# Kernel optimization log

Hardware: AMD Instinct MI355X
Metric: run time of the kernel (lower is better)

Reference implementation:

```python
import jax, jax.numpy as jnp
import numpy as np

N_U, N_P, E, E_LAB = 100000, 50000, 2000000, 500000
D_U, D_P, H = 64, 128, 64


def _seg_mean(feat, idx, n):
    # scatter-mean: sum per destination / clamp(count, 1)
    s = jax.ops.segment_sum(feat, idx, num_segments=n)
    c = jax.ops.segment_sum(jnp.ones((idx.shape[0],), feat.dtype), idx, num_segments=n)
    return s / jnp.maximum(c, 1.0)[:, None]


def setup_inputs() -> dict:
    key = jax.random.key(0)
    ks = jax.random.split(key, 16)
    inp = {
        'x_user': jax.random.normal(ks[0], (N_U, D_U), jnp.float32),
        'x_product': jax.random.normal(ks[1], (N_P, D_P), jnp.float32),
        'W1_buys_l': jax.random.normal(ks[2], (D_U, H), jnp.float32) * 0.05,
        'b1_buys': jnp.zeros((H,), jnp.float32),
        'W1_buys_r': jax.random.normal(ks[3], (D_P, H), jnp.float32) * 0.05,
        'W1_rev_l': jax.random.normal(ks[4], (D_P, H), jnp.float32) * 0.05,
        'b1_rev': jnp.zeros((H,), jnp.float32),
        'W1_rev_r': jax.random.normal(ks[5], (D_U, H), jnp.float32) * 0.05,
        'W2_buys_l': jax.random.normal(ks[6], (H, H), jnp.float32) * 0.05,
        'b2_buys': jnp.zeros((H,), jnp.float32),
        'W2_buys_r': jax.random.normal(ks[7], (H, H), jnp.float32) * 0.05,
        'W2_rev_l': jax.random.normal(ks[8], (H, H), jnp.float32) * 0.05,
        'b2_rev': jnp.zeros((H,), jnp.float32),
        'W2_rev_r': jax.random.normal(ks[9], (H, H), jnp.float32) * 0.05,
        'edge_src': jax.random.randint(ks[10], (E,), 0, N_U, jnp.int32),
        'edge_dst': jax.random.randint(ks[11], (E,), 0, N_P, jnp.int32),
        'lab_u': jax.random.randint(ks[12], (E_LAB,), 0, N_U, jnp.int32),
        'lab_p': jax.random.randint(ks[13], (E_LAB,), 0, N_P, jnp.int32),
    }
    return inp


def reference(x_user, x_product, W1_buys_l, b1_buys, W1_buys_r, W1_rev_l, b1_rev, W1_rev_r,
              W2_buys_l, b2_buys, W2_buys_r, W2_rev_l, b2_rev, W2_rev_r,
              edge_src, edge_dst, lab_u, lab_p):
    # SAGEConv (mean aggr): out_dst = mean_agg(x_src) @ W_l + b + x_dst @ W_r
    def sage(x_src, x_dst, src, dst, n_dst, Wl, b, Wr):
        agg = _seg_mean(x_src[src], dst, n_dst)
        return agg @ Wl + b + x_dst @ Wr

    n_u, n_p = x_user.shape[0], x_product.shape[0]
    # layer 1 (per edge type, hetero) + relu
    h_p = jax.nn.relu(sage(x_user, x_product, edge_src, edge_dst, n_p, W1_buys_l, b1_buys, W1_buys_r))
    h_u = jax.nn.relu(sage(x_product, x_user, edge_dst, edge_src, n_u, W1_rev_l, b1_rev, W1_rev_r))
    # layer 2
    h_p2 = sage(h_u, h_p, edge_src, edge_dst, n_p, W2_buys_l, b2_buys, W2_buys_r)
    h_u2 = sage(h_p, h_u, edge_dst, edge_src, n_u, W2_rev_l, b2_rev, W2_rev_r)
    # classifier: per-label-edge dot product
    return jnp.sum(h_u2[lab_u] * h_p2[lab_p], axis=-1)
```

## Files before the change

### kernel.cpp

```cpp
#include <hip/hip_runtime.h>


using u16 = unsigned short;
using u32 = unsigned int;

__device__ __forceinline__ u16 bf16r(float f) {
    u32 b = __float_as_uint(f);
    b += 0x7fffu + ((b >> 16) & 1u);
    return (u16)(b >> 16);
}
__device__ __forceinline__ float bflo(u32 u) { return __uint_as_float(u << 16); }
__device__ __forceinline__ float bfhi(u32 u) { return __uint_as_float(u & 0xffff0000u); }

#define BSH 8
#define MAXB 512
#define CHUNK 4096
#define RPT 16
#define HB 512

__global__ __launch_bounds__(256) void k_histCast(const int* __restrict__ esrc,
                                                  const int* __restrict__ edst,
                                                  int* __restrict__ bcntP,
                                                  int* __restrict__ bcntU,
                                                  int NBP, int NBU, int E,
                                                  const float* __restrict__ xc,
                                                  u16* __restrict__ yc, int n8) {
    __shared__ int hP[MAXB];
    __shared__ int hU[MAXB];
    int tid = threadIdx.x;
    if ((int)blockIdx.x >= HB) {
        int i = (blockIdx.x - HB) * 256 + tid;
        if (i < n8) {
            const float4* x4 = (const float4*)xc;
            float4 a = x4[i * 2], b = x4[i * 2 + 1];
            uint4 o;
            o.x = (u32)bf16r(a.x) | ((u32)bf16r(a.y) << 16);
            o.y = (u32)bf16r(a.z) | ((u32)bf16r(a.w) << 16);
            o.z = (u32)bf16r(b.x) | ((u32)bf16r(b.y) << 16);
            o.w = (u32)bf16r(b.z) | ((u32)bf16r(b.w) << 16);
            ((uint4*)yc)[i] = o;
        }
        return;
    }
    for (int i = tid; i < MAXB; i += 256) { hP[i] = 0; hU[i] = 0; }
    __syncthreads();
    int E4 = E >> 2;
    const int4* s4 = (const int4*)esrc;
    const int4* d4 = (const int4*)edst;
    int stride = HB * 256;
    for (int i = blockIdx.x * 256 + tid; i < E4; i += stride) {
        int4 s = s4[i], d = d4[i];
        atomicAdd(&hU[s.x >> BSH], 1); atomicAdd(&hU[s.y >> BSH], 1);
        atomicAdd(&hU[s.z >> BSH], 1); atomicAdd(&hU[s.w >> BSH], 1);
        atomicAdd(&hP[d.x >> BSH], 1); atomicAdd(&hP[d.y >> BSH], 1);
        atomicAdd(&hP[d.z >> BSH], 1); atomicAdd(&hP[d.w >> BSH], 1);
    }
    if (blockIdx.x == 0 && tid < (E & 3)) {
        int e = E4 * 4 + tid;
        atomicAdd(&hU[esrc[e] >> BSH], 1);
        atomicAdd(&hP[edst[e] >> BSH], 1);
    }
    __syncthreads();
    for (int i = tid; i < NBP; i += 256) if (hP[i]) atomicAdd(&bcntP[i], hP[i]);
    for (int i = tid; i < NBU; i += 256) if (hU[i]) atomicAdd(&bcntU[i], hU[i]);
}

__global__ __launch_bounds__(256) void k_scanBuckets(const int* __restrict__ cntP,
                                                     int* __restrict__ basesP,
                                                     int* __restrict__ curP, int NBP,
                                                     const int* __restrict__ cntU,
                                                     int* __restrict__ basesU,
                                                     int* __restrict__ curU, int NBU) {
    const int* cnt; int* bases; int* cur; int NB;
    if (blockIdx.x == 0) { cnt = cntP; bases = basesP; cur = curP; NB = NBP; }
    else                 { cnt = cntU; bases = basesU; cur = curU; NB = NBU; }
    __shared__ int sA[MAXB];
    __shared__ int sB[MAXB];
    int tid = threadIdx.x;
    int v0 = (tid < NB) ? cnt[tid] : 0;
    int v1 = (tid + 256 < NB) ? cnt[tid + 256] : 0;
    sA[tid] = v0; sA[tid + 256] = v1;
    __syncthreads();
    int* src = sA; int* dst = sB;
    for (int off = 1; off < MAXB; off <<= 1) {
        dst[tid] = src[tid] + ((tid >= off) ? src[tid - off] : 0);
        int i2 = tid + 256;
        dst[i2] = src[i2] + ((i2 >= off) ? src[i2 - off] : 0);
        __syncthreads();
        int* t = src; src = dst; dst = t;
    }
    if (tid < NB)       { bases[tid] = src[tid] - v0;             cur[tid] = src[tid] - v0; }
    if (tid + 256 < NB) { bases[tid + 256] = src[tid + 256] - v1; cur[tid + 256] = src[tid + 256] - v1; }
    if (tid == 0) bases[NB] = src[MAXB - 1];
}

__global__ __launch_bounds__(256) void k_partition2(
    const int* __restrict__ keysP, const int* __restrict__ payP,
    int* __restrict__ curPp, uint2* __restrict__ pairsP, int NBP,
    const int* __restrict__ keysU, const int* __restrict__ payU,
    int* __restrict__ curUp, uint2* __restrict__ pairsU, int NBU,
    int E, int pblocks) {
    __shared__ int hist[MAXB];
    __shared__ int sA[MAXB];
    __shared__ int sB[MAXB];
    __shared__ int bx[MAXB];
    __shared__ int gbase[MAXB];
    __shared__ uint2 prs[CHUNK];
    const int* keys; const int* payload; int* cursor; uint2* pairs; int NB, cb;
    if ((int)blockIdx.x < pblocks) {
        keys = keysP; payload = payP; cursor = curPp; pairs = pairsP; NB = NBP;
        cb = blockIdx.x;
    } else {
        keys = keysU; payload = payU; cursor = curUp; pairs = pairsU; NB = NBU;
        cb = blockIdx.x - pblocks;
    }
    int tid = threadIdx.x;
    int i0 = cb * CHUNK;
    int count = min(CHUNK, E - i0);
    for (int i = tid; i < MAXB; i += 256) hist[i] = 0;
    __syncthreads();
    int keyr[RPT], payr[RPT], rankr[RPT];
#pragma unroll
    for (int r = 0; r < RPT; ++r) {
        int idx = r * 256 + tid;
        if (idx < count) {
            int k = keys[i0 + idx];
            keyr[r] = k;
            payr[r] = payload[i0 + idx];
            rankr[r] = atomicAdd(&hist[k >> BSH], 1);
        } else keyr[r] = -1;
    }
    __syncthreads();
    sA[tid] = hist[tid]; sA[tid + 256] = hist[tid + 256];
    __syncthreads();
    int* src = sA; int* dst = sB;
    for (int off = 1; off < MAXB; off <<= 1) {
        dst[tid] = src[tid] + ((tid >= off) ? src[tid - off] : 0);
        int i2 = tid + 256;
        dst[i2] = src[i2] + ((i2 >= off) ? src[i2 - off] : 0);
        __syncthreads();
        int* t = src; src = dst; dst = t;
    }
    bx[tid] = src[tid] - hist[tid];
    bx[tid + 256] = src[tid + 256] - hist[tid + 256];
    __syncthreads();
    for (int b = tid; b < NB; b += 256) {
        int c = hist[b];
        gbase[b] = c ? atomicAdd(&cursor[b], c) : 0;
    }
#pragma unroll
    for (int r = 0; r < RPT; ++r) {
        if (keyr[r] >= 0)
            prs[bx[keyr[r] >> BSH] + rankr[r]] = make_uint2((u32)keyr[r], (u32)payr[r]);
    }
    __syncthreads();
    for (int j = tid; j < count; j += 256) {
        uint2 pr = prs[j];
        int b = pr.x >> BSH;
        pairs[gbase[b] + (j - bx[b])] = pr;
    }
}

__global__ __launch_bounds__(256) void k_bucketFill(
    const uint2* __restrict__ pairsP, const int* __restrict__ basesP, int NBP,
    int* __restrict__ nbr_p, int* __restrict__ deg_p, int* __restrict__ ptr_p, int NP,
    const uint2* __restrict__ pairsU, const int* __restrict__ basesU, int NBU,
    int* __restrict__ nbr_u, int* __restrict__ deg_u, int* __restrict__ ptr_u, int NU) {
    const uint2* pairs; const int* bases; int* nbr; int* deg; int* ptr; int N; int bucket;
    if ((int)blockIdx.x < NBP) {
        pairs = pairsP; bases = basesP; nbr = nbr_p; deg = deg_p; ptr = ptr_p; N = NP;
        bucket = blockIdx.x;
    } else {
        pairs = pairsU; bases = basesU; nbr = nbr_u; deg = deg_u; ptr = ptr_u; N = NU;
        bucket = blockIdx.x - NBP;
    }
    int tid = threadIdx.x;
    int base = bases[bucket];
    int cnt = bases[bucket + 1] - base;
    __shared__ int h[256];
    __shared__ int s[256];
    __shared__ int cur[256];
    h[tid] = 0;
    __syncthreads();
    for (int j = tid; j < cnt; j += 256) atomicAdd(&h[pairs[base + j].x & 255], 1);
    __syncthreads();
    int d = h[tid];
    s[tid] = d;
    __syncthreads();
    for (int off = 1; off < 256; off <<= 1) {
        int v = (tid >= off) ? s[tid - off] : 0;
        __syncthreads();
        s[tid] += v;
        __syncthreads();
    }
    int excl = s[tid] - d;
    int node = bucket * 256 + tid;
    if (node < N) { deg[node] = d; ptr[node] = base + excl; }
    cur[tid] = excl;
    __syncthreads();
    for (int j = tid; j < cnt; j += 256) {
        uint2 pr = pairs[base + j];
        int pos = atomicAdd(&cur[pr.x & 255], 1);
        nbr[base + pos] = (int)(pr.y << 7);
    }
}

#define ACC8(A0,A1,A2,A3,A4,A5,A6,A7,V) \
    A0 += bflo((V).x); A1 += bfhi((V).x); A2 += bflo((V).y); A3 += bfhi((V).y); \
    A4 += bflo((V).z); A5 += bfhi((V).z); A6 += bflo((V).w); A7 += bfhi((V).w);

__global__ __launch_bounds__(256) void k_gather2(
    const u16* __restrict__ yA, const int* __restrict__ nbrA, const int* __restrict__ stpA,
    const int* __restrict__ degA, float* __restrict__ aggA, int NA,
    const u16* __restrict__ yB, const int* __restrict__ nbrB, const int* __restrict__ stpB,
    const int* __restrict__ degB, float* __restrict__ aggB, int NB) {
    int w = (blockIdx.x * 256 + threadIdx.x) >> 6;
    int lane = threadIdx.x & 63;
    if (w >= NA + NB) return;
    const u16* y; const int* nbr; const int* stp; const int* deg; float* agg; int n;
    if (w < NA) { y = yA; nbr = nbrA; stp = stpA; deg = degA; agg = aggA; n = w; }
    else        { y = yB; nbr = nbrB; stp = stpB; deg = degB; agg = aggB; n = w - NA; }
    const int q = lane >> 3, t = lane & 7;
    const int d = deg[n];
    const int st = stp[n];
    const char* yb = (const char*)y + t * 16;
    float a0=0,a1=0,a2=0,a3=0,a4=0,a5=0,a6=0,a7=0;
    for (int j = 0; j < d; j += 64) {
        const int cnt = min(d - j, 64);
        int offv = 0;
        if (lane < cnt) offv = nbr[st + j + lane];
#define GLD(R) \
        int g##R = __shfl(offv, R * 8 + q, 64); \
        uint4 v##R = make_uint4(0u, 0u, 0u, 0u); \
        if (R * 8 + q < cnt) v##R = *(const uint4*)(yb + g##R);
        GLD(0) GLD(1) GLD(2) GLD(3) GLD(4) GLD(5) GLD(6) GLD(7)
#undef GLD
#define ACCR(R) if (R * 8 < cnt) { ACC8(a0,a1,a2,a3,a4,a5,a6,a7,v##R) }
        ACCR(0) ACCR(1) ACCR(2) ACCR(3) ACCR(4) ACCR(5) ACCR(6) ACCR(7)
#undef ACCR
    }
#pragma unroll
    for (int m = 8; m < 64; m <<= 1) {
        a0 += __shfl_xor(a0, m, 64); a1 += __shfl_xor(a1, m, 64);
        a2 += __shfl_xor(a2, m, 64); a3 += __shfl_xor(a3, m, 64);
        a4 += __shfl_xor(a4, m, 64); a5 += __shfl_xor(a5, m, 64);
        a6 += __shfl_xor(a6, m, 64); a7 += __shfl_xor(a7, m, 64);
    }
    if (q == 0) {
        float dinv = 1.0f / (float)max(d, 1);
        float* dstp = agg + n * 64 + t * 8;
        *(float4*)dstp       = make_float4(a0 * dinv, a1 * dinv, a2 * dinv, a3 * dinv);
        *(float4*)(dstp + 4) = make_float4(a4 * dinv, a5 * dinv, a6 * dinv, a7 * dinv);
    }
}

#define FMA_ROW(ACC, O, W4) \
    ACC[0] += (O) * (W4).x; ACC[1] += (O) * (W4).y; \
    ACC[2] += (O) * (W4).z; ACC[3] += (O) * (W4).w;

template <int K, int ROWS, bool RELU, bool EMIT, bool PRE, bool BIAS, bool STORE>
__global__ __launch_bounds__(256) void k_ctile(const float* __restrict__ pre,
                                               const float* __restrict__ bias,
                                               const float* __restrict__ x,
                                               const float* __restrict__ W,
                                               float* __restrict__ h,
                                               u16* __restrict__ hbf, int N) {
    constexpr int RR = ROWS / 16;
    constexpr int STRIDE = K + 4;
    constexpr int KF4 = K / 4;
    __shared__ float Ws[K * 64];
    __shared__ float op[ROWS * STRIDE];
    const int tid = threadIdx.x;
    for (int i = tid; i < K * 16; i += 256)
        ((float4*)Ws)[i] = ((const float4*)W)[i];
    const int c4 = (tid & 15) * 4;
    const int rb = (tid >> 4) * RR;
    float bx_ = 0.f, by_ = 0.f, bz_ = 0.f, bw_ = 0.f;
    if (BIAS) {
        float4 b4 = *(const float4*)(bias + c4);
        bx_ = b4.x; by_ = b4.y; bz_ = b4.z; bw_ = b4.w;
    }
    const int ntiles = (N + ROWS - 1) / ROWS;
    for (int tile = blockIdx.x; tile < ntiles; tile += gridDim.x) {
        const int row0 = tile * ROWS;
        __syncthreads();
        for (int i = tid; i < ROWS * KF4; i += 256) {
            int r = i / KF4, k4 = (i % KF4) * 4;
            int row = row0 + r;
            float4 v = make_float4(0.f, 0.f, 0.f, 0.f);
            if (row < N) v = *(const float4*)(x + (size_t)row * K + k4);
            *(float4*)(op + r * STRIDE + k4) = v;
        }
        __syncthreads();
        float acc[RR][4];
#pragma unroll
        for (int i = 0; i < RR; ++i) {
            float px = 0.f, py = 0.f, pz = 0.f, pw = 0.f;
            if (PRE) {
                int row = row0 + rb + i;
                if (row < N) {
                    float4 p = *(const float4*)(pre + row * 64 + c4);
                    px = p.x; py = p.y; pz = p.z; pw = p.w;
                }
            }
            acc[i][0] = bx_ + px; acc[i][1] = by_ + py;
            acc[i][2] = bz_ + pz; acc[i][3] = bw_ + pw;
        }
        for (int kk = 0; kk < K; kk += 4) {
            float4 w0 = *(const float4*)(Ws + (kk + 0) * 64 + c4);
            float4 w1 = *(const float4*)(Ws + (kk + 1) * 64 + c4);
            float4 w2 = *(const float4*)(Ws + (kk + 2) * 64 + c4);
            float4 w3 = *(const float4*)(Ws + (kk + 3) * 64 + c4);
#pragma unroll
            for (int i = 0; i < RR; ++i) {
                float4 o = *(const float4*)(op + (rb + i) * STRIDE + kk);
                FMA_ROW(acc[i], o.x, w0);
                FMA_ROW(acc[i], o.y, w1);
                FMA_ROW(acc[i], o.z, w2);
                FMA_ROW(acc[i], o.w, w3);
            }
        }
#pragma unroll
        for (int i = 0; i < RR; ++i) {
            int row = row0 + rb + i;
            if (row >= N) continue;
            float v0 = acc[i][0], v1 = acc[i][1], v2 = acc[i][2], v3 = acc[i][3];
            if (RELU) {
                v0 = fmaxf(v0, 0.f); v1 = fmaxf(v1, 0.f);
                v2 = fmaxf(v2, 0.f); v3 = fmaxf(v3, 0.f);
            }
            if (STORE)
                *(float4*)(h + row * 64 + c4) = make_float4(v0, v1, v2, v3);
            if (EMIT) {
                uint2 o;
                o.x = (u32)bf16r(v0) | ((u32)bf16r(v1) << 16);
                o.y = (u32)bf16r(v2) | ((u32)bf16r(v3) << 16);
                *(uint2*)(hbf + row * 64 + c4) = o;
            }
        }
    }
}

template <bool PRE, bool BIAS, bool RELU, bool EMIT>
__global__ __launch_bounds__(256) void k_ctilePair64X(
    const float* __restrict__ pre0, const float* __restrict__ bias0,
    const float* __restrict__ x0, const float* __restrict__ W0,
    float* __restrict__ h0, u16* __restrict__ hbf0, int N0, int g0,
    const float* __restrict__ pre1, const float* __restrict__ bias1,
    const float* __restrict__ x1, const float* __restrict__ W1,
    float* __restrict__ h1, u16* __restrict__ hbf1, int N1) {
    constexpr int ROWS = 64, RR = 4, STRIDE = 68, KF4 = 16;
    __shared__ float Ws[64 * 64];
    __shared__ float op[ROWS * STRIDE];
    const float* pre; const float* bias; const float* x; const float* W;
    float* h; u16* hbf;
    int N, bid, gsz;
    if ((int)blockIdx.x < g0) {
        pre = pre0; bias = bias0; x = x0; W = W0; h = h0; hbf = hbf0; N = N0;
        bid = blockIdx.x; gsz = g0;
    } else {
        pre = pre1; bias = bias1; x = x1; W = W1; h = h1; hbf = hbf1; N = N1;
        bid = blockIdx.x - g0; gsz = gridDim.x - g0;
    }
    const int tid = threadIdx.x;
    for (int i = tid; i < 64 * 16; i += 256)
        ((float4*)Ws)[i] = ((const float4*)W)[i];
    const int c4 = (tid & 15) * 4;
    const int rb = (tid >> 4) * RR;
    float bx_ = 0.f, by_ = 0.f, bz_ = 0.f, bw_ = 0.f;
    if (BIAS) {
        float4 b4 = *(const float4*)(bias + c4);
        bx_ = b4.x; by_ = b4.y; bz_ = b4.z; bw_ = b4.w;
    }
    const int ntiles = (N + ROWS - 1) / ROWS;
    for (int tile = bid; tile < ntiles; tile += gsz) {
        const int row0 = tile * ROWS;
        __syncthreads();
        for (int i = tid; i < ROWS * KF4; i += 256) {
            int r = i / KF4, k4 = (i % KF4) * 4;
            int row = row0 + r;
            float4 v = make_float4(0.f, 0.f, 0.f, 0.f);
            if (row < N) v = *(const float4*)(x + (size_t)row * 64 + k4);
            *(float4*)(op + r * STRIDE + k4) = v;
        }
        __syncthreads();
        float acc[RR][4];
#pragma unroll
        for (int i = 0; i < RR; ++i) {
            float px = 0.f, py = 0.f, pz = 0.f, pw = 0.f;
            if (PRE) {
                int row = row0 + rb + i;
                if (row < N) {
                    float4 p = *(const float4*)(pre + row * 64 + c4);
                    px = p.x; py = p.y; pz = p.z; pw = p.w;
                }
            }
            acc[i][0] = bx_ + px; acc[i][1] = by_ + py;
            acc[i][2] = bz_ + pz; acc[i][3] = bw_ + pw;
        }
        for (int kk = 0; kk < 64; kk += 4) {
            float4 w0 = *(const float4*)(Ws + (kk + 0) * 64 + c4);
            float4 w1 = *(const float4*)(Ws + (kk + 1) * 64 + c4);
            float4 w2 = *(const float4*)(Ws + (kk + 2) * 64 + c4);
            float4 w3 = *(const float4*)(Ws + (kk + 3) * 64 + c4);
#pragma unroll
            for (int i = 0; i < RR; ++i) {
                float4 o = *(const float4*)(op + (rb + i) * STRIDE + kk);
                FMA_ROW(acc[i], o.x, w0);
                FMA_ROW(acc[i], o.y, w1);
                FMA_ROW(acc[i], o.z, w2);
                FMA_ROW(acc[i], o.w, w3);
            }
        }
#pragma unroll
        for (int i = 0; i < RR; ++i) {
            int row = row0 + rb + i;
            if (row >= N) continue;
            float v0 = acc[i][0], v1 = acc[i][1], v2 = acc[i][2], v3 = acc[i][3];
            if (RELU) {
                v0 = fmaxf(v0, 0.f); v1 = fmaxf(v1, 0.f);
                v2 = fmaxf(v2, 0.f); v3 = fmaxf(v3, 0.f);
            }
            *(float4*)(h + row * 64 + c4) = make_float4(v0, v1, v2, v3);
            if (EMIT) {
                uint2 o;
                o.x = (u32)bf16r(v0) | ((u32)bf16r(v1) << 16);
                o.y = (u32)bf16r(v2) | ((u32)bf16r(v3) << 16);
                *(uint2*)(hbf + row * 64 + c4) = o;
            }
        }
    }
}

template <bool BIAS>
__global__ __launch_bounds__(256) void k_ctilePairCat(
    const float* __restrict__ bias0, const float* __restrict__ xa0,
    const float* __restrict__ xb0, const float* __restrict__ Wa0,
    const float* __restrict__ Wb0, float* __restrict__ h0, int N0, int g0,
    const float* __restrict__ bias1, const float* __restrict__ xa1,
    const float* __restrict__ xb1, const float* __restrict__ Wa1,
    const float* __restrict__ Wb1, float* __restrict__ h1, int N1) {
    constexpr int ROWS = 32, RR = 2, STRIDE = 132, KF4 = 32;
    __shared__ float Ws[128 * 64];
    __shared__ float op[ROWS * STRIDE];
    const float* bias; const float* xa; const float* xb;
    const float* Wa; const float* Wb; float* h;
    int N, bid, gsz;
    if ((int)blockIdx.x < g0) {
        bias = bias0; xa = xa0; xb = xb0; Wa = Wa0; Wb = Wb0; h = h0; N = N0;
        bid = blockIdx.x; gsz = g0;
    } else {
        bias = bias1; xa = xa1; xb = xb1; Wa = Wa1; Wb = Wb1; h = h1; N = N1;
        bid = blockIdx.x - g0; gsz = gridDim.x - g0;
    }
    const int tid = threadIdx.x;
    for (int i = tid; i < 64 * 16; i += 256) {
        ((float4*)Ws)[i]           = ((const float4*)Wa)[i];
        ((float4*)Ws)[64 * 16 + i] = ((const float4*)Wb)[i];
    }
    const int c4 = (tid & 15) * 4;
    const int rb = (tid >> 4) * RR;
    float bx_ = 0.f, by_ = 0.f, bz_ = 0.f, bw_ = 0.f;
    if (BIAS) {
        float4 b4 = *(const float4*)(bias + c4);
        bx_ = b4.x; by_ = b4.y; bz_ = b4.z; bw_ = b4.w;
    }
    const int ntiles = (N + ROWS - 1) / ROWS;
    for (int tile = bid; tile < ntiles; tile += gsz) {
        const int row0 = tile * ROWS;
        __syncthreads();
        for (int i = tid; i < ROWS * KF4; i += 256) {
            int r = i >> 5, k4 = (i & 31) * 4;
            int row = row0 + r;
            float4 v = make_float4(0.f, 0.f, 0.f, 0.f);
            if (row < N)
                v = (k4 < 64) ? *(const float4*)(xa + (size_t)row * 64 + k4)
                              : *(const float4*)(xb + (size_t)row * 64 + (k4 - 64));
            *(float4*)(op + r * STRIDE + k4) = v;
        }
        __syncthreads();
        float acc[RR][4];
#pragma unroll
        for (int i = 0; i < RR; ++i) {
            acc[i][0] = bx_; acc[i][1] = by_; acc[i][2] = bz_; acc[i][3] = bw_;
        }
        for (int kk = 0; kk < 128; kk += 4) {
            float4 w0 = *(const float4*)(Ws + (kk + 0) * 64 + c4);
            float4 w1 = *(const float4*)(Ws + (kk + 1) * 64 + c4);
            float4 w2 = *(const float4*)(Ws + (kk + 2) * 64 + c4);
            float4 w3 = *(const float4*)(Ws + (kk + 3) * 64 + c4);
#pragma unroll
            for (int i = 0; i < RR; ++i) {
                float4 o = *(const float4*)(op + (rb + i) * STRIDE + kk);
                FMA_ROW(acc[i], o.x, w0);
                FMA_ROW(acc[i], o.y, w1);
                FMA_ROW(acc[i], o.z, w2);
                FMA_ROW(acc[i], o.w, w3);
            }
        }
#pragma unroll
        for (int i = 0; i < RR; ++i) {
            int row = row0 + rb + i;
            if (row >= N) continue;
            *(float4*)(h + row * 64 + c4) =
                make_float4(acc[i][0], acc[i][1], acc[i][2], acc[i][3]);
        }
    }
}

__global__ __launch_bounds__(256) void k_classify4(const float* __restrict__ hu,
                                                   const float* __restrict__ hp,
                                                   const int* __restrict__ lu,
                                                   const int* __restrict__ lp,
                                                   float* __restrict__ out, int EL) {
    int w = (blockIdx.x * 256 + threadIdx.x) >> 6;
    int lane = threadIdx.x & 63;
    int q = lane >> 4, t = lane & 15;
    int e = w * 4 + q;
    float v = 0.f;
    if (e < EL) {
        int u = lu[e], p = lp[e];
        float4 a = *(const float4*)(hu + u * 64 + t * 4);
        float4 b = *(const float4*)(hp + p * 64 + t * 4);
        v = a.x * b.x + a.y * b.y + a.z * b.z + a.w * b.w;
    }
#pragma unroll
    for (int m = 1; m < 16; m <<= 1) v += __shfl_xor(v, m, 64);
    if (t == 0 && e < EL) out[e] = v;
}

extern "C" void kernel_launch(void* const* d_in, const int* in_sizes, int n_in,
                              void* d_out, int out_size, void* d_ws, size_t ws_size,
                              hipStream_t stream) {
    const float* x_user    = (const float*)d_in[0];
    const float* x_product = (const float*)d_in[1];
    const float* W1bl = (const float*)d_in[2];
    const float* b1b  = (const float*)d_in[3];
    const float* W1br = (const float*)d_in[4];
    const float* W1rl = (const float*)d_in[5];
    const float* b1r  = (const float*)d_in[6];
    const float* W1rr = (const float*)d_in[7];
    const float* W2bl = (const float*)d_in[8];
    const float* b2b  = (const float*)d_in[9];
    const float* W2br = (const float*)d_in[10];
    const float* W2rl = (const float*)d_in[11];
    const float* b2r  = (const float*)d_in[12];
    const float* W2rr = (const float*)d_in[13];
    const int* esrc = (const int*)d_in[14];
    const int* edst = (const int*)d_in[15];
    const int* lu   = (const int*)d_in[16];
    const int* lp   = (const int*)d_in[17];

    const int NU = in_sizes[0] / 64;
    const int NP = in_sizes[1] / 128;
    const int E  = in_sizes[14];
    const int EL = in_sizes[16];
    const int NBP = (NP + 255) >> BSH;
    const int NBU = (NU + 255) >> BSH;

    char* ws = (char*)d_ws;
    size_t off = 0;
    auto alloc = [&](size_t bytes) -> void* {
        void* p = ws + off;
        off += (bytes + 255) & ~(size_t)255;
        return p;
    };
    int*   deg_u  = (int*)alloc((size_t)NU * 4);
    int*   deg_p  = (int*)alloc((size_t)NP * 4);
    int*   ptr_u  = (int*)alloc((size_t)NU * 4);
    int*   ptr_p  = (int*)alloc((size_t)NP * 4);
    int*   bcntP  = (int*)alloc((size_t)MAXB * 4);
    int*   bcntU  = (int*)alloc((size_t)MAXB * 4);
    int*   basesP = (int*)alloc((size_t)(MAXB + 1) * 4);
    int*   basesU = (int*)alloc((size_t)(MAXB + 1) * 4);
    int*   curP   = (int*)alloc((size_t)MAXB * 4);
    int*   curU   = (int*)alloc((size_t)MAXB * 4);
    int*   nbr_u  = (int*)alloc((size_t)E * 4);
    int*   nbr_p  = (int*)alloc((size_t)E * 4);
    size_t aggBytes = (size_t)(NP + NU) * 64 * 4;
    size_t pairBytes = (size_t)E * 8 * 2;
    char* uni = (char*)alloc(aggBytes > pairBytes ? aggBytes : pairBytes);
    float* aggP   = (float*)uni;
    float* aggU   = (float*)(uni + (size_t)NP * 64 * 4);
    uint2* pairsP = (uint2*)uni;
    uint2* pairsU = (uint2*)(uni + (size_t)E * 8);
    u16*   bfA    = (u16*)alloc((size_t)NU * 64 * 2);
    u16*   bfB    = (u16*)alloc((size_t)NP * 64 * 2);
    float* h_p    = (float*)alloc((size_t)NP * 64 * 4);
    float* h_u    = (float*)alloc((size_t)NU * 64 * 4);

    hipMemsetAsync(bcntP, 0, (size_t)MAXB * 2 * 4, stream);
    const int n8 = NU * 64 / 8;
    const int castBlocks = (n8 + 255) / 256;
    k_histCast<<<HB + castBlocks, 256, 0, stream>>>(esrc, edst, bcntP, bcntU, NBP, NBU, E,
                                                    x_user, bfA, n8);
    k_scanBuckets<<<2, 256, 0, stream>>>(bcntP, basesP, curP, NBP, bcntU, basesU, curU, NBU);
    const int pblocks = (E + CHUNK - 1) / CHUNK;
    k_partition2<<<2 * pblocks, 256, 0, stream>>>(edst, esrc, curP, pairsP, NBP,
                                                  esrc, edst, curU, pairsU, NBU, E, pblocks);
    k_bucketFill<<<NBP + NBU, 256, 0, stream>>>(pairsP, basesP, NBP, nbr_p, deg_p, ptr_p, NP,
                                                pairsU, basesU, NBU, nbr_u, deg_u, ptr_u, NU);

    const int tP32 = (NP + 31) / 32;
    const int tP64 = (NP + 63) / 64, tU64 = (NU + 63) / 64;
    const int tU32 = (NU + 31) / 32;
    auto cap = [](int t, int c) { return t < c ? t : c; };

    k_ctile<128, 32, false, true, false, false, false><<<cap(tP32, 768), 256, 0, stream>>>(
        nullptr, nullptr, x_product, W1rl, nullptr, bfB, NP);
    k_ctile<128, 32, false, false, false, false, true><<<cap(tP32, 768), 256, 0, stream>>>(
        nullptr, nullptr, x_product, W1br, h_p, nullptr, NP);

    k_gather2<<<(NP + NU + 3) / 4, 256, 0, stream>>>(bfA, nbr_p, ptr_p, deg_p, aggP, NP,
                                                     bfB, nbr_u, ptr_u, deg_u, aggU, NU);
    {
        const int gP = cap(tP64, 512), gU = cap(tU64, 1024);
        k_ctilePair64X<true, true, true, true><<<gP + gU, 256, 0, stream>>>(
            h_p, b1b, aggP, W1bl, h_p, bfB, NP, gP,
            aggU, b1r, x_user, W1rr, h_u, bfA, NU);
    }

    k_gather2<<<(NP + NU + 3) / 4, 256, 0, stream>>>(bfA, nbr_p, ptr_p, deg_p, aggP, NP,
                                                     bfB, nbr_u, ptr_u, deg_u, aggU, NU);
    {
        const int gP = cap(tP32, 512), gU = cap(tU32, 1024);
        k_ctilePairCat<true><<<gP + gU, 256, 0, stream>>>(
            b2b, aggP, h_p, W2bl, W2br, h_p, NP, gP,
            b2r, aggU, h_u, W2rl, W2rr, h_u, NU);
    }

    k_classify4<<<((EL + 3) / 4 + 3) / 4, 256, 0, stream>>>(h_u, h_p, lu, lp, (float*)d_out, EL);
}
```

Measured before the change: 497.6 us.

## Bucket-sort label edges by product and merge the two layer-1 projection launches

Label edges are bucket-partitioned by product index using the existing histogram, scan and partition pipeline. The classifier then walks them in sorted order so h_p gathers hit cache better, and writes outputs through the stored original index. The two K=128 projection kernels on x_product become one paired launch via a generalized k_ctilePairX template, with sink buffers absorbing the unused outputs. This adds sorting work, an extra pairs buffer and scattered output writes in exchange for better locality and fewer launches.

```diff
diff --git a/kernel.cpp b/kernel.cpp
--- a/kernel.cpp
+++ b/kernel.cpp
@@ -17,19 +17,24 @@
 #define CHUNK 4096
 #define RPT 16
 #define HB 512
+#define LB 64
 
 __global__ __launch_bounds__(256) void k_histCast(const int* __restrict__ esrc,
                                                   const int* __restrict__ edst,
                                                   int* __restrict__ bcntP,
                                                   int* __restrict__ bcntU,
                                                   int NBP, int NBU, int E,
+                                                  const int* __restrict__ labp,
+                                                  int* __restrict__ bcntL,
+                                                  int NBL, int EL,
                                                   const float* __restrict__ xc,
                                                   u16* __restrict__ yc, int n8) {
     __shared__ int hP[MAXB];
     __shared__ int hU[MAXB];
     int tid = threadIdx.x;
-    if ((int)blockIdx.x >= HB) {
-        int i = (blockIdx.x - HB) * 256 + tid;
+    int bix = blockIdx.x;
+    if (bix >= HB + LB) {
+        int i = (bix - HB - LB) * 256 + tid;
         if (i < n8) {
             const float4* x4 = (const float4*)xc;
             float4 a = x4[i * 2], b = x4[i * 2 + 1];
@@ -42,20 +47,37 @@
         }
         return;
     }
+    if (bix >= HB) {
+        for (int i = tid; i < MAXB; i += 256) hP[i] = 0;
+        __syncthreads();
+        int EL4 = EL >> 2;
+        const int4* l4 = (const int4*)labp;
+        int stride = LB * 256;
+        for (int i = (bix - HB) * 256 + tid; i < EL4; i += stride) {
+            int4 l = l4[i];
+            atomicAdd(&hP[l.x >> BSH], 1); atomicAdd(&hP[l.y >> BSH], 1);
+            atomicAdd(&hP[l.z >> BSH], 1); atomicAdd(&hP[l.w >> BSH], 1);
+        }
+        if (bix == HB && tid < (EL & 3))
+            atomicAdd(&hP[labp[EL4 * 4 + tid] >> BSH], 1);
+        __syncthreads();
+        for (int i = tid; i < NBL; i += 256) if (hP[i]) atomicAdd(&bcntL[i], hP[i]);
+        return;
+    }
     for (int i = tid; i < MAXB; i += 256) { hP[i] = 0; hU[i] = 0; }
     __syncthreads();
     int E4 = E >> 2;
     const int4* s4 = (const int4*)esrc;
     const int4* d4 = (const int4*)edst;
     int stride = HB * 256;
-    for (int i = blockIdx.x * 256 + tid; i < E4; i += stride) {
+    for (int i = bix * 256 + tid; i < E4; i += stride) {
         int4 s = s4[i], d = d4[i];
         atomicAdd(&hU[s.x >> BSH], 1); atomicAdd(&hU[s.y >> BSH], 1);
         atomicAdd(&hU[s.z >> BSH], 1); atomicAdd(&hU[s.w >> BSH], 1);
         atomicAdd(&hP[d.x >> BSH], 1); atomicAdd(&hP[d.y >> BSH], 1);
         atomicAdd(&hP[d.z >> BSH], 1); atomicAdd(&hP[d.w >> BSH], 1);
     }
-    if (blockIdx.x == 0 && tid < (E & 3)) {
+    if (bix == 0 && tid < (E & 3)) {
         int e = E4 * 4 + tid;
         atomicAdd(&hU[esrc[e] >> BSH], 1);
         atomicAdd(&hP[edst[e] >> BSH], 1);
@@ -70,10 +92,14 @@
                                                      int* __restrict__ curP, int NBP,
                                                      const int* __restrict__ cntU,
                                                      int* __restrict__ basesU,
-                                                     int* __restrict__ curU, int NBU) {
+                                                     int* __restrict__ curU, int NBU,
+                                                     const int* __restrict__ cntL,
+                                                     int* __restrict__ basesL,
+                                                     int* __restrict__ curL, int NBL) {
     const int* cnt; int* bases; int* cur; int NB;
-    if (blockIdx.x == 0) { cnt = cntP; bases = basesP; cur = curP; NB = NBP; }
-    else                 { cnt = cntU; bases = basesU; cur = curU; NB = NBU; }
+    if (blockIdx.x == 0)      { cnt = cntP; bases = basesP; cur = curP; NB = NBP; }
+    else if (blockIdx.x == 1) { cnt = cntU; bases = basesU; cur = curU; NB = NBU; }
+    else                      { cnt = cntL; bases = basesL; cur = curL; NB = NBL; }
     __shared__ int sA[MAXB];
     __shared__ int sB[MAXB];
     int tid = threadIdx.x;
@@ -94,29 +120,34 @@
     if (tid == 0) bases[NB] = src[MAXB - 1];
 }
 
-__global__ __launch_bounds__(256) void k_partition2(
+__global__ __launch_bounds__(256) void k_partition3(
     const int* __restrict__ keysP, const int* __restrict__ payP,
     int* __restrict__ curPp, uint2* __restrict__ pairsP, int NBP,
     const int* __restrict__ keysU, const int* __restrict__ payU,
     int* __restrict__ curUp, uint2* __restrict__ pairsU, int NBU,
-    int E, int pblocks) {
+    int E, int pblocks,
+    const int* __restrict__ keysL,
+    int* __restrict__ curLp, uint2* __restrict__ pairsL, int NBL, int EL) {
     __shared__ int hist[MAXB];
     __shared__ int sA[MAXB];
     __shared__ int sB[MAXB];
     __shared__ int bx[MAXB];
     __shared__ int gbase[MAXB];
     __shared__ uint2 prs[CHUNK];
-    const int* keys; const int* payload; int* cursor; uint2* pairs; int NB, cb;
+    const int* keys; const int* pay; int* cursor; uint2* pairs; int NB, cb, nE;
     if ((int)blockIdx.x < pblocks) {
-        keys = keysP; payload = payP; cursor = curPp; pairs = pairsP; NB = NBP;
-        cb = blockIdx.x;
+        keys = keysP; pay = payP; cursor = curPp; pairs = pairsP; NB = NBP;
+        cb = blockIdx.x; nE = E;
+    } else if ((int)blockIdx.x < 2 * pblocks) {
+        keys = keysU; pay = payU; cursor = curUp; pairs = pairsU; NB = NBU;
+        cb = blockIdx.x - pblocks; nE = E;
     } else {
-        keys = keysU; payload = payU; cursor = curUp; pairs = pairsU; NB = NBU;
-        cb = blockIdx.x - pblocks;
+        keys = keysL; pay = nullptr; cursor = curLp; pairs = pairsL; NB = NBL;
+        cb = blockIdx.x - 2 * pblocks; nE = EL;
     }
     int tid = threadIdx.x;
     int i0 = cb * CHUNK;
-    int count = min(CHUNK, E - i0);
+    int count = min(CHUNK, nE - i0);
     for (int i = tid; i < MAXB; i += 256) hist[i] = 0;
     __syncthreads();
     int keyr[RPT], payr[RPT], rankr[RPT];
@@ -126,7 +157,7 @@
         if (idx < count) {
             int k = keys[i0 + idx];
             keyr[r] = k;
-            payr[r] = payload[i0 + idx];
+            payr[r] = pay ? pay[i0 + idx] : (i0 + idx);
             rankr[r] = atomicAdd(&hist[k >> BSH], 1);
         } else keyr[r] = -1;
     }
@@ -258,18 +289,30 @@
     ACC[0] += (O) * (W4).x; ACC[1] += (O) * (W4).y; \
     ACC[2] += (O) * (W4).z; ACC[3] += (O) * (W4).w;
 
-template <int K, int ROWS, bool RELU, bool EMIT, bool PRE, bool BIAS, bool STORE>
-__global__ __launch_bounds__(256) void k_ctile(const float* __restrict__ pre,
-                                               const float* __restrict__ bias,
-                                               const float* __restrict__ x,
-                                               const float* __restrict__ W,
-                                               float* __restrict__ h,
-                                               u16* __restrict__ hbf, int N) {
+template <int K, bool PRE, bool BIAS, bool RELU, bool EMIT>
+__global__ __launch_bounds__(256) void k_ctilePairX(
+    const float* __restrict__ pre0, const float* __restrict__ bias0,
+    const float* __restrict__ x0, const float* __restrict__ W0,
+    float* __restrict__ h0, u16* __restrict__ hbf0, int N0, int g0,
+    const float* __restrict__ pre1, const float* __restrict__ bias1,
+    const float* __restrict__ x1, const float* __restrict__ W1,
+    float* __restrict__ h1, u16* __restrict__ hbf1, int N1) {
+    constexpr int ROWS = (K == 64) ? 64 : 32;
     constexpr int RR = ROWS / 16;
     constexpr int STRIDE = K + 4;
     constexpr int KF4 = K / 4;
     __shared__ float Ws[K * 64];
     __shared__ float op[ROWS * STRIDE];
+    const float* pre; const float* bias; const float* x; const float* W;
+    float* h; u16* hbf;
+    int N, bid, gsz;
+    if ((int)blockIdx.x < g0) {
+        pre = pre0; bias = bias0; x = x0; W = W0; h = h0; hbf = hbf0; N = N0;
+        bid = blockIdx.x; gsz = g0;
+    } else {
+        pre = pre1; bias = bias1; x = x1; W = W1; h = h1; hbf = hbf1; N = N1;
+        bid = blockIdx.x - g0; gsz = gridDim.x - g0;
+    }
     const int tid = threadIdx.x;
     for (int i = tid; i < K * 16; i += 256)
         ((float4*)Ws)[i] = ((const float4*)W)[i];
@@ -281,7 +324,7 @@
         bx_ = b4.x; by_ = b4.y; bz_ = b4.z; bw_ = b4.w;
     }
     const int ntiles = (N + ROWS - 1) / ROWS;
-    for (int tile = blockIdx.x; tile < ntiles; tile += gridDim.x) {
+    for (int tile = bid; tile < ntiles; tile += gsz) {
         const int row0 = tile * ROWS;
         __syncthreads();
         for (int i = tid; i < ROWS * KF4; i += 256) {
@@ -307,98 +350,6 @@
             acc[i][2] = bz_ + pz; acc[i][3] = bw_ + pw;
         }
         for (int kk = 0; kk < K; kk += 4) {
-            float4 w0 = *(const float4*)(Ws + (kk + 0) * 64 + c4);
-            float4 w1 = *(const float4*)(Ws + (kk + 1) * 64 + c4);
-            float4 w2 = *(const float4*)(Ws + (kk + 2) * 64 + c4);
-            float4 w3 = *(const float4*)(Ws + (kk + 3) * 64 + c4);
-#pragma unroll
-            for (int i = 0; i < RR; ++i) {
-                float4 o = *(const float4*)(op + (rb + i) * STRIDE + kk);
-                FMA_ROW(acc[i], o.x, w0);
-                FMA_ROW(acc[i], o.y, w1);
-                FMA_ROW(acc[i], o.z, w2);
-                FMA_ROW(acc[i], o.w, w3);
-            }
-        }
-#pragma unroll
-        for (int i = 0; i < RR; ++i) {
-            int row = row0 + rb + i;
-            if (row >= N) continue;
-            float v0 = acc[i][0], v1 = acc[i][1], v2 = acc[i][2], v3 = acc[i][3];
-            if (RELU) {
-                v0 = fmaxf(v0, 0.f); v1 = fmaxf(v1, 0.f);
-                v2 = fmaxf(v2, 0.f); v3 = fmaxf(v3, 0.f);
-            }
-            if (STORE)
-                *(float4*)(h + row * 64 + c4) = make_float4(v0, v1, v2, v3);
-            if (EMIT) {
-                uint2 o;
-                o.x = (u32)bf16r(v0) | ((u32)bf16r(v1) << 16);
-                o.y = (u32)bf16r(v2) | ((u32)bf16r(v3) << 16);
-                *(uint2*)(hbf + row * 64 + c4) = o;
-            }
-        }
-    }
-}
-
-template <bool PRE, bool BIAS, bool RELU, bool EMIT>
-__global__ __launch_bounds__(256) void k_ctilePair64X(
-    const float* __restrict__ pre0, const float* __restrict__ bias0,
-    const float* __restrict__ x0, const float* __restrict__ W0,
-    float* __restrict__ h0, u16* __restrict__ hbf0, int N0, int g0,
-    const float* __restrict__ pre1, const float* __restrict__ bias1,
-    const float* __restrict__ x1, const float* __restrict__ W1,
-    float* __restrict__ h1, u16* __restrict__ hbf1, int N1) {
-    constexpr int ROWS = 64, RR = 4, STRIDE = 68, KF4 = 16;
-    __shared__ float Ws[64 * 64];
-    __shared__ float op[ROWS * STRIDE];
-    const float* pre; const float* bias; const float* x; const float* W;
-    float* h; u16* hbf;
-    int N, bid, gsz;
-    if ((int)blockIdx.x < g0) {
-        pre = pre0; bias = bias0; x = x0; W = W0; h = h0; hbf = hbf0; N = N0;
-        bid = blockIdx.x; gsz = g0;
-    } else {
-        pre = pre1; bias = bias1; x = x1; W = W1; h = h1; hbf = hbf1; N = N1;
-        bid = blockIdx.x - g0; gsz = gridDim.x - g0;
-    }
-    const int tid = threadIdx.x;
-    for (int i = tid; i < 64 * 16; i += 256)
-        ((float4*)Ws)[i] = ((const float4*)W)[i];
-    const int c4 = (tid & 15) * 4;
-    const int rb = (tid >> 4) * RR;
-    float bx_ = 0.f, by_ = 0.f, bz_ = 0.f, bw_ = 0.f;
-    if (BIAS) {
-        float4 b4 = *(const float4*)(bias + c4);
-        bx_ = b4.x; by_ = b4.y; bz_ = b4.z; bw_ = b4.w;
-    }
-    const int ntiles = (N + ROWS - 1) / ROWS;
-    for (int tile = bid; tile < ntiles; tile += gsz) {
-        const int row0 = tile * ROWS;
-        __syncthreads();
-        for (int i = tid; i < ROWS * KF4; i += 256) {
-            int r = i / KF4, k4 = (i % KF4) * 4;
-            int row = row0 + r;
-            float4 v = make_float4(0.f, 0.f, 0.f, 0.f);
-            if (row < N) v = *(const float4*)(x + (size_t)row * 64 + k4);
-            *(float4*)(op + r * STRIDE + k4) = v;
-        }
-        __syncthreads();
-        float acc[RR][4];
-#pragma unroll
-        for (int i = 0; i < RR; ++i) {
-            float px = 0.f, py = 0.f, pz = 0.f, pw = 0.f;
-            if (PRE) {
-                int row = row0 + rb + i;
-                if (row < N) {
-                    float4 p = *(const float4*)(pre + row * 64 + c4);
-                    px = p.x; py = p.y; pz = p.z; pw = p.w;
-                }
-            }
-            acc[i][0] = bx_ + px; acc[i][1] = by_ + py;
-            acc[i][2] = bz_ + pz; acc[i][3] = bw_ + pw;
-        }
-        for (int kk = 0; kk < 64; kk += 4) {
             float4 w0 = *(const float4*)(Ws + (kk + 0) * 64 + c4);
             float4 w1 = *(const float4*)(Ws + (kk + 1) * 64 + c4);
             float4 w2 = *(const float4*)(Ws + (kk + 2) * 64 + c4);
@@ -508,25 +459,30 @@
     }
 }
 
-__global__ __launch_bounds__(256) void k_classify4(const float* __restrict__ hu,
+__global__ __launch_bounds__(256) void k_classifyS(const float* __restrict__ hu,
                                                    const float* __restrict__ hp,
                                                    const int* __restrict__ lu,
-                                                   const int* __restrict__ lp,
+                                                   const uint2* __restrict__ pairsL,
                                                    float* __restrict__ out, int EL) {
     int w = (blockIdx.x * 256 + threadIdx.x) >> 6;
     int lane = threadIdx.x & 63;
     int q = lane >> 4, t = lane & 15;
-    int e = w * 4 + q;
+    int j = w * 4 + q;
     float v = 0.f;
-    if (e < EL) {
-        int u = lu[e], p = lp[e];
-        float4 a = *(const float4*)(hu + u * 64 + t * 4);
-        float4 b = *(const float4*)(hp + p * 64 + t * 4);
+    int e = 0;
+    bool ok = j < EL;
+    if (ok) {
+        uint2 pr = pairsL[j];
+        int p = (int)pr.x;
+        e = (int)pr.y;
+        int u = lu[e];
+        float4 a = *(const float4*)(hu + (size_t)u * 64 + t * 4);
+        float4 b = *(const float4*)(hp + (size_t)p * 64 + t * 4);
         v = a.x * b.x + a.y * b.y + a.z * b.z + a.w * b.w;
     }
 #pragma unroll
     for (int m = 1; m < 16; m <<= 1) v += __shfl_xor(v, m, 64);
-    if (t == 0 && e < EL) out[e] = v;
+    if (t == 0 && ok) out[e] = v;
 }
 
 extern "C" void kernel_launch(void* const* d_in, const int* in_sizes, int n_in,
@@ -557,6 +513,7 @@
     const int EL = in_sizes[16];
     const int NBP = (NP + 255) >> BSH;
     const int NBU = (NU + 255) >> BSH;
+    const int NBL = NBP;
 
     char* ws = (char*)d_ws;
     size_t off = 0;
@@ -571,12 +528,16 @@
     int*   ptr_p  = (int*)alloc((size_t)NP * 4);
     int*   bcntP  = (int*)alloc((size_t)MAXB * 4);
     int*   bcntU  = (int*)alloc((size_t)MAXB * 4);
+    int*   bcntL  = (int*)alloc((size_t)MAXB * 4);
     int*   basesP = (int*)alloc((size_t)(MAXB + 1) * 4);
     int*   basesU = (int*)alloc((size_t)(MAXB + 1) * 4);
+    int*   basesL = (int*)alloc((size_t)(MAXB + 1) * 4);
     int*   curP   = (int*)alloc((size_t)MAXB * 4);
     int*   curU   = (int*)alloc((size_t)MAXB * 4);
+    int*   curL   = (int*)alloc((size_t)MAXB * 4);
     int*   nbr_u  = (int*)alloc((size_t)E * 4);
     int*   nbr_p  = (int*)alloc((size_t)E * 4);
+    uint2* pairsL = (uint2*)alloc((size_t)EL * 8);
     size_t aggBytes = (size_t)(NP + NU) * 64 * 4;
     size_t pairBytes = (size_t)E * 8 * 2;
     char* uni = (char*)alloc(aggBytes > pairBytes ? aggBytes : pairBytes);
@@ -588,34 +549,44 @@
     u16*   bfB    = (u16*)alloc((size_t)NP * 64 * 2);
     float* h_p    = (float*)alloc((size_t)NP * 64 * 4);
     float* h_u    = (float*)alloc((size_t)NU * 64 * 4);
-
-    hipMemsetAsync(bcntP, 0, (size_t)MAXB * 2 * 4, stream);
+    float* sinkF  = h_u;
+    u16*   sinkB  = (u16*)((char*)h_u + (size_t)NP * 64 * 4);
+
+    hipMemsetAsync(bcntP, 0, (size_t)MAXB * 3 * 4, stream);
     const int n8 = NU * 64 / 8;
     const int castBlocks = (n8 + 255) / 256;
-    k_histCast<<<HB + castBlocks, 256, 0, stream>>>(esrc, edst, bcntP, bcntU, NBP, NBU, E,
-                                                    x_user, bfA, n8);
-    k_scanBuckets<<<2, 256, 0, stream>>>(bcntP, basesP, curP, NBP, bcntU, basesU, curU, NBU);
+    k_histCast<<<HB + LB + castBlocks, 256, 0, stream>>>(
+        esrc, edst, bcntP, bcntU, NBP, NBU, E,
+        lp, bcntL, NBL, EL, x_user, bfA, n8);
+    k_scanBuckets<<<3, 256, 0, stream>>>(bcntP, basesP, curP, NBP,
+                                         bcntU, basesU, curU, NBU,
+                                         bcntL, basesL, curL, NBL);
     const int pblocks = (E + CHUNK - 1) / CHUNK;
-    k_partition2<<<2 * pblocks, 256, 0, stream>>>(edst, esrc, curP, pairsP, NBP,
-                                                  esrc, edst, curU, pairsU, NBU, E, pblocks);
+    const int lblocks = (EL + CHUNK - 1) / CHUNK;
+    k_partition3<<<2 * pblocks + lblocks, 256, 0, stream>>>(
+        edst, esrc, curP, pairsP, NBP,
+        esrc, edst, curU, pairsU, NBU, E, pblocks,
+        lp, curL, pairsL, NBL, EL);
     k_bucketFill<<<NBP + NBU, 256, 0, stream>>>(pairsP, basesP, NBP, nbr_p, deg_p, ptr_p, NP,
                                                 pairsU, basesU, NBU, nbr_u, deg_u, ptr_u, NU);
 
     const int tP32 = (NP + 31) / 32;
+    const int tU32 = (NU + 31) / 32;
     const int tP64 = (NP + 63) / 64, tU64 = (NU + 63) / 64;
-    const int tU32 = (NU + 31) / 32;
     auto cap = [](int t, int c) { return t < c ? t : c; };
 
-    k_ctile<128, 32, false, true, false, false, false><<<cap(tP32, 768), 256, 0, stream>>>(
-        nullptr, nullptr, x_product, W1rl, nullptr, bfB, NP);
-    k_ctile<128, 32, false, false, false, false, true><<<cap(tP32, 768), 256, 0, stream>>>(
-        nullptr, nullptr, x_product, W1br, h_p, nullptr, NP);
+    {
+        const int g0 = cap(tP32, 768);
+        k_ctilePairX<128, false, false, false, true><<<g0 + cap(tP32, 768), 256, 0, stream>>>(
+            nullptr, nullptr, x_product, W1rl, sinkF, bfB, NP, g0,
+            nullptr, nullptr, x_product, W1br, h_p, sinkB, NP);
+    }
 
     k_gather2<<<(NP + NU + 3) / 4, 256, 0, stream>>>(bfA, nbr_p, ptr_p, deg_p, aggP, NP,
                                                      bfB, nbr_u, ptr_u, deg_u, aggU, NU);
     {
         const int gP = cap(tP64, 512), gU = cap(tU64, 1024);
-        k_ctilePair64X<true, true, true, true><<<gP + gU, 256, 0, stream>>>(
+        k_ctilePairX<64, true, true, true, true><<<gP + gU, 256, 0, stream>>>(
             h_p, b1b, aggP, W1bl, h_p, bfB, NP, gP,
             aggU, b1r, x_user, W1rr, h_u, bfA, NU);
     }
@@ -629,5 +600,6 @@
             b2r, aggU, h_u, W2rl, W2rr, h_u, NU);
     }
 
-    k_classify4<<<((EL + 3) / 4 + 3) / 4, 256, 0, stream>>>(h_u, h_p, lu, lp, (float*)d_out, EL);
-}
+    k_classifyS<<<((EL + 3) / 4 + 3) / 4, 256, 0, stream>>>(h_u, h_p, lu, pairsL,
+                                                            (float*)d_out, EL);
+}
```

After: 492.3 us. About the same (-1.1%).
